# Kernel tuning notes

Hardware: AMD Instinct MI355X
Metric: run time of the kernel (lower is better)

The kernel has to match this reference:

```python
import jax, jax.numpy as jnp
import numpy as np

EMB = 1024

def setup_inputs() -> dict:
    key = jax.random.key(0)
    ks = jax.random.split(key, 6)
    B, S, E = 4, 2048, EMB
    x = jax.random.normal(ks[0], (B, S, E), dtype=jnp.float32)
    attention_mask = jax.random.randint(ks[1], (B, S, S), 0, 2, dtype=jnp.int32)
    proj_w = jax.random.normal(ks[2], (E, 3 * E), dtype=jnp.float32) * (1.0 / np.sqrt(E))
    proj_b = jax.random.normal(ks[3], (3 * E,), dtype=jnp.float32) * 0.02
    out_w = jax.random.normal(ks[4], (E, E), dtype=jnp.float32) * (1.0 / np.sqrt(E))
    out_b = jax.random.normal(ks[5], (E,), dtype=jnp.float32) * 0.02
    return {"x": x, "attention_mask": attention_mask, "proj_w": proj_w,
            "proj_b": proj_b, "out_w": out_w, "out_b": out_b}

def reference(x, attention_mask, proj_w, proj_b, out_w, out_b):
    E = x.shape[-1]
    scale = 1.0 / jnp.sqrt(jnp.asarray(E, x.dtype))
    qkv = x @ proj_w + proj_b                      # [B,S,3E]
    q, k, v = jnp.split(qkv, 3, axis=-1)           # each [B,S,E]
    scores = jnp.einsum('bqe,bke->bqk', q, k) * scale  # [B,S,S]
    scores = jnp.where(attention_mask == 0, jnp.asarray(-1e20, scores.dtype), scores)
    attn = jax.nn.softmax(scores, axis=-1)
    ctx = jnp.einsum('bqk,bke->bqe', attn, v)      # [B,S,E]
    return ctx @ out_w + out_b
```

## Files before the change

kernel.cpp:

```cpp
#include <hip/hip_runtime.h>
#include <cstdint>

typedef unsigned short u16;
typedef uint32_t u32;
typedef __bf16 bf16x8 __attribute__((ext_vector_type(8)));
typedef float f32x4 __attribute__((ext_vector_type(4)));

__device__ __forceinline__ u16 f2bf(float f) {
  unsigned u = __float_as_uint(f);
  u += 0x7fffu + ((u >> 16) & 1u);
  return (u16)(u >> 16);
}

__device__ __forceinline__ void async16(const void* g, void* l) {
  __builtin_amdgcn_global_load_lds(
      (const __attribute__((address_space(1))) uint32_t*)g,
      (__attribute__((address_space(3))) uint32_t*)l, 16, 0, 0);
}

__global__ __launch_bounds__(256) void k_prep(const float* __restrict__ x, u16* __restrict__ xb,
                                              const float* __restrict__ pw, u16* __restrict__ wt,
                                              const float* __restrict__ ow, u16* __restrict__ owt,
                                              const int* __restrict__ mask, u32* __restrict__ mbits) {
  const int bid = blockIdx.x;
  if (bid < 8192) {
    const int i = bid * 256 + threadIdx.x;
    const float4 v = ((const float4*)x)[i];
    ushort4 o;
    o.x = f2bf(v.x); o.y = f2bf(v.y); o.z = f2bf(v.z); o.w = f2bf(v.w);
    ((ushort4*)xb)[i] = o;
    return;
  }
  if (bid >= 12288) {
    const size_t w = (size_t)(bid - 12288) * 256 + threadIdx.x;
    const int* p = mask + w * 32;
    u32 bits = 0;
#pragma unroll
    for (int j = 0; j < 8; ++j) {
      const int4 v = ((const int4*)p)[j];
      bits |= (u32)(v.x & 1) << (j * 4 + 0);
      bits |= (u32)(v.y & 1) << (j * 4 + 1);
      bits |= (u32)(v.z & 1) << (j * 4 + 2);
      bits |= (u32)(v.w & 1) << (j * 4 + 3);
    }
    mbits[w] = bits;
    return;
  }
  __shared__ u16 tile[32][33];
  const int tx = threadIdx.x & 31, ty = threadIdx.x >> 5;
  const float* in;
  u16* outp;
  int lda, ldo, c0, r0;
  if (bid < 11264) {
    const int id = bid - 8192;
    c0 = (id % 96) * 32; r0 = (id / 96) * 32;
    in = pw; outp = wt; lda = 3072; ldo = 1024;
  } else {
    const int id = bid - 11264;
    c0 = (id % 32) * 32; r0 = (id / 32) * 32;
    in = ow; outp = owt; lda = 1024; ldo = 1024;
  }
#pragma unroll
  for (int i = 0; i < 4; ++i)
    tile[ty + i * 8][tx] = f2bf(in[(size_t)(r0 + ty + i * 8) * lda + c0 + tx]);
  __syncthreads();
#pragma unroll
  for (int i = 0; i < 4; ++i)
    outp[(size_t)(c0 + ty + i * 8) * ldo + r0 + tx] = tile[tx][ty + i * 8];
}

template <int MODE, int TM, int BN>
__device__ __forceinline__ void gemm_core(
    u16* As, u16* Bs,
    const u16* __restrict__ A, long lda, long bsA,
    const u16* __restrict__ Bt, long ldb, long bsB,
    void* __restrict__ C, long ldc, long bsC,
    int M, int N, int K,
    const float* __restrict__ bias, const u32* __restrict__ mbits,
    int b, int bx, int by) {
  constexpr int MT = TM / 32, NT = BN / 32;
  constexpr int ACALLS = TM / 8, TOT = (TM + BN) / 8, NC = TOT / 4;
  const int m0 = by * TM, n0 = bx * BN;
  const int lane = threadIdx.x & 63;
  const int w = threadIdx.x >> 6;
  const int wr = w >> 1, wc = w & 1;

  const int srow = lane >> 3;
  const int scol = ((lane & 7) ^ ((lane >> 3) & 7)) * 8;
  const u16* pa = A + (size_t)b * bsA + (size_t)(m0 + srow) * lda + scol;
  const u16* pb = Bt + (size_t)b * bsB + (size_t)(n0 + srow) * ldb + scol;

  const int m_l = lane & 15, q = lane >> 4, m7 = m_l & 7;
  const int offs[2] = {(q ^ m7) * 8, ((4 + q) ^ m7) * 8};

  f32x4 acc[MT][NT] = {};
  f32x4 accs[MT] = {};
  bf16x8 ones;
#pragma unroll
  for (int e = 0; e < 8; ++e) ones[e] = (__bf16)1.0f;

  for (int kt = 0; kt < K; kt += 64) {
    __syncthreads();
#pragma unroll
    for (int g = 0; g < NC; ++g) {
      const int idx = w * NC + g;
      if (idx < ACALLS)
        async16(pa + (size_t)(idx * 8) * lda, As + idx * 512);
      else
        async16(pb + (size_t)((idx - ACALLS) * 8) * ldb, Bs + (idx - ACALLS) * 512);
    }
    __syncthreads();
#pragma unroll
    for (int s = 0; s < 2; ++s) {
      bf16x8 af[MT], bfr[NT];
#pragma unroll
      for (int t = 0; t < MT; ++t)
        af[t] = *(const bf16x8*)(As + (wr * (TM / 2) + t * 16 + m_l) * 64 + offs[s]);
#pragma unroll
      for (int t = 0; t < NT; ++t)
        bfr[t] = *(const bf16x8*)(Bs + (wc * (BN / 2) + t * 16 + m_l) * 64 + offs[s]);
#pragma unroll
      for (int mt = 0; mt < MT; ++mt)
#pragma unroll
        for (int nt = 0; nt < NT; ++nt)
          acc[mt][nt] = __builtin_amdgcn_mfma_f32_16x16x32_bf16(af[mt], bfr[nt], acc[mt][nt], 0, 0, 0);
      if constexpr (MODE == 2) {
#pragma unroll
        for (int mt = 0; mt < MT; ++mt)
          accs[mt] = __builtin_amdgcn_mfma_f32_16x16x32_bf16(af[mt], ones, accs[mt], 0, 0, 0);
      }
    }
    pa += 64;
    pb += 64;
  }

  if constexpr (MODE == 1) {
    __syncthreads();
    const int rl = threadIdx.x >> 1, pr = threadIdx.x & 1;
    const uint2 v = *(const uint2*)(mbits + ((size_t)(b * M + m0 + rl)) * (N >> 5) + (n0 >> 5) + pr * 2);
    ((u32*)As)[rl * 4 + pr * 2] = v.x;
    ((u32*)As)[rl * 4 + pr * 2 + 1] = v.y;
    __syncthreads();
  }

  float rinv[MT][4];
  if constexpr (MODE == 2) {
#pragma unroll
    for (int mt = 0; mt < MT; ++mt)
#pragma unroll
      for (int r = 0; r < 4; ++r) rinv[mt][r] = 1.0f / accs[mt][r];
  }

#pragma unroll
  for (int mt = 0; mt < MT; ++mt) {
#pragma unroll
    for (int nt = 0; nt < NT; ++nt) {
      const int col = n0 + wc * (BN / 2) + nt * 16 + m_l;
      const int row0 = m0 + wr * (TM / 2) + mt * 16 + q * 4;
      if constexpr (MODE == 3) {
        ushort4 o;
        o.x = f2bf(acc[mt][nt][0]); o.y = f2bf(acc[mt][nt][1]);
        o.z = f2bf(acc[mt][nt][2]); o.w = f2bf(acc[mt][nt][3]);
        *(ushort4*)((u16*)C + (size_t)b * bsC + (size_t)col * ldc + row0) = o;
      } else {
#pragma unroll
        for (int r = 0; r < 4; ++r) {
          const int row = row0 + r;
          float v = acc[mt][nt][r];
          if constexpr (MODE == 0) {
            v += bias[col];
            if (col < 1024) v *= 0.03125f;
            ((u16*)C)[(size_t)b * bsC + (size_t)row * ldc + col] = f2bf(v);
          } else if constexpr (MODE == 1) {
            const int cl = wc * 64 + nt * 16 + m_l;
            const int rl = wr * 64 + mt * 16 + q * 4 + r;
            const u32 wb = ((const u32*)As)[rl * 4 + (cl >> 5)];
            v = ((wb >> (cl & 31)) & 1u) ? __expf(fminf(v, 30.f)) : 0.f;
            ((u16*)C)[(size_t)b * bsC + (size_t)row * ldc + col] = f2bf(v);
          } else if constexpr (MODE == 2) {
            v = v * rinv[mt][r] + bias[col];
            ((float*)C)[(size_t)b * bsC + (size_t)row * ldc + col] = v;
          }
        }
      }
    }
  }
}

template <int MODE, int TM, int BN>
__global__ __launch_bounds__(256) void gemm_bt(
    const u16* __restrict__ A, long lda, long bsA,
    const u16* __restrict__ Bt, long ldb, long bsB,
    void* __restrict__ C, long ldc, long bsC,
    int M, int N, int K,
    const float* __restrict__ bias, const u32* __restrict__ mbits) {
  __shared__ u16 As[TM * 64];
  __shared__ u16 Bs[BN * 64];
  const int gx = gridDim.x, gxy = gridDim.x * gridDim.y;
  const int T = gxy * gridDim.z;
  int L = blockIdx.x + gx * blockIdx.y + gxy * blockIdx.z;
  L = (L & 7) * (T >> 3) + (L >> 3);
  const int bz = L / gxy, r = L % gxy;
  gemm_core<MODE, TM, BN>(As, Bs, A, lda, bsA, Bt, ldb, bsB, C, ldc, bsC, M, N, K,
                          bias, mbits, bz, r % gx, r / gx);
}

extern "C" void kernel_launch(void* const* d_in, const int* in_sizes, int n_in,
                              void* d_out, int out_size, void* d_ws, size_t ws_size,
                              hipStream_t stream) {
  const float* x = (const float*)d_in[0];
  const int* mask = (const int*)d_in[1];
  const float* proj_w = (const float*)d_in[2];
  const float* proj_b = (const float*)d_in[3];
  const float* out_w = (const float*)d_in[4];
  const float* out_b = (const float*)d_in[5];
  float* out = (float*)d_out;

  char* ws = (char*)d_ws;
  u16* xb = (u16*)(ws);
  u16* wt = (u16*)(ws + 16777216);
  u16* owt = (u16*)(ws + 23068672);
  u16* qkv = (u16*)(ws + 25165824);
  u16* P = (u16*)(ws + 75497472);
  u32* mbits = (u32*)(ws + 109051904);
  u16* Ut = (u16*)xb;

  k_prep<<<14336, 256, 0, stream>>>(x, xb, proj_w, wt, out_w, owt, mask, mbits);
  gemm_bt<0, 128, 128><<<dim3(24, 64, 1), 256, 0, stream>>>(
      xb, 1024, 0, wt, 1024, 0, qkv, 3072, 0, 8192, 3072, 1024, proj_b, nullptr);
  gemm_bt<1, 128, 128><<<dim3(16, 16, 4), 256, 0, stream>>>(
      qkv, 3072, (long)2048 * 3072, qkv + 1024, 3072, (long)2048 * 3072,
      P, 2048, (long)2048 * 2048, 2048, 2048, 1024, nullptr, mbits);
  gemm_bt<3, 64, 128><<<dim3(8, 32, 4), 256, 0, stream>>>(
      qkv + 2048, 3072, (long)2048 * 3072, owt, 1024, 0,
      Ut, 2048, (long)1024 * 2048, 2048, 1024, 1024, nullptr, nullptr);
  gemm_bt<2, 128, 128><<<dim3(8, 16, 4), 256, 0, stream>>>(
      P, 2048, (long)2048 * 2048, Ut, 2048, (long)1024 * 2048,
      out, 1024, (long)2048 * 1024, 2048, 1024, 2048, out_b, nullptr);
}
```

Before: 331.7 us.

## Add 256x256 multi-stage pipelined GEMM for QKV projection and score kernels

```diff
diff --git a/kernel.cpp b/kernel.cpp
--- a/kernel.cpp
+++ b/kernel.cpp
@@ -67,6 +67,120 @@
 #pragma unroll
   for (int i = 0; i < 4; ++i)
     outp[(size_t)(c0 + ty + i * 8) * ldo + r0 + tx] = tile[tx][ty + i * 8];
+}
+
+template <int MODE>
+__global__ __launch_bounds__(512, 2) void gemm256(
+    const u16* __restrict__ A, long lda, long bsA,
+    const u16* __restrict__ Bt, long ldb, long bsB,
+    void* __restrict__ C, long ldc, long bsC,
+    int M, int N, int K,
+    const float* __restrict__ bias, const u32* __restrict__ mbits) {
+  __shared__ u16 sm[4][2][8192];
+  const int gx = gridDim.x, gxy = gridDim.x * gridDim.y;
+  const int T = gxy * gridDim.z;
+  int L = blockIdx.x + gx * blockIdx.y + gxy * blockIdx.z;
+  L = (L & 7) * (T >> 3) + (L >> 3);
+  const int b = L / gxy, rr = L % gxy, bx = rr % gx, by = rr / gx;
+  const int m0 = by * 256, n0 = bx * 256;
+  const int tid = threadIdx.x;
+  const int lane = tid & 63;
+  const int w = tid >> 6;
+  const int wr = w >> 2, wc = w & 3;
+
+  const int srow = tid >> 2;
+  const int sg = ((tid & 3) ^ (srow & 3)) * 8;
+  const u16* pa = A + (size_t)b * bsA + (size_t)(m0 + srow) * lda + sg;
+  const u16* pb = Bt + (size_t)b * bsB + (size_t)(n0 + srow) * ldb + sg;
+  const size_t a128 = (size_t)128 * lda, b128 = (size_t)128 * ldb;
+
+  const int m_l = lane & 15, q = lane >> 4;
+  const int xg = (q ^ (m_l & 3)) * 8;
+  const int aoff = (wr * 128 + m_l) * 32 + xg;
+  const int boff = (wc * 64 + m_l) * 32 + xg;
+
+  f32x4 acc[8][4] = {};
+
+#define STAGE(tt)                                   \
+  {                                                 \
+    const int bi_ = (tt)&3;                         \
+    const size_t ko_ = (size_t)(tt)*32;             \
+    u16* da_ = &sm[bi_][0][0] + tid * 8;            \
+    u16* db_ = &sm[bi_][1][0] + tid * 8;            \
+    async16(pa + ko_, da_);                         \
+    async16(pa + ko_ + a128, da_ + 4096);           \
+    async16(pb + ko_, db_);                         \
+    async16(pb + ko_ + b128, db_ + 4096);           \
+  }
+
+  const int NTL = K >> 5;
+  STAGE(0) STAGE(1) STAGE(2)
+  asm volatile("s_waitcnt vmcnt(8)" ::: "memory");
+  __builtin_amdgcn_s_barrier();
+
+  for (int t = 0; t < NTL; ++t) {
+    const u16* ab = &sm[t & 3][0][0] + aoff;
+    const u16* bb = &sm[t & 3][1][0] + boff;
+    bf16x8 af[8], bf[4];
+#pragma unroll
+    for (int mt = 0; mt < 8; ++mt) af[mt] = *(const bf16x8*)(ab + mt * 512);
+#pragma unroll
+    for (int nt = 0; nt < 4; ++nt) bf[nt] = *(const bf16x8*)(bb + nt * 512);
+    if (t + 3 < NTL) STAGE(t + 3)
+    __builtin_amdgcn_s_setprio(1);
+#pragma unroll
+    for (int mt = 0; mt < 8; ++mt)
+#pragma unroll
+      for (int nt = 0; nt < 4; ++nt)
+        acc[mt][nt] = __builtin_amdgcn_mfma_f32_16x16x32_bf16(af[mt], bf[nt], acc[mt][nt], 0, 0, 0);
+    __builtin_amdgcn_s_setprio(0);
+    __builtin_amdgcn_sched_barrier(0);
+    if (t + 3 < NTL)
+      asm volatile("s_waitcnt vmcnt(8)" ::: "memory");
+    else if (t + 3 == NTL)
+      asm volatile("s_waitcnt vmcnt(4)" ::: "memory");
+    else if (t + 2 == NTL)
+      asm volatile("s_waitcnt vmcnt(0)" ::: "memory");
+    if (t + 1 < NTL) __builtin_amdgcn_s_barrier();
+  }
+#undef STAGE
+
+  if constexpr (MODE == 1) {
+    __syncthreads();
+    u32* smw = (u32*)&sm[0][0][0];
+    const int rl = tid >> 1, wo = (tid & 1) * 4;
+    const uint4 mv = *(const uint4*)(mbits + ((size_t)b * M + m0 + rl) * (N >> 5) + (n0 >> 5) + wo);
+    smw[rl * 8 + wo] = mv.x;
+    smw[rl * 8 + wo + 1] = mv.y;
+    smw[rl * 8 + wo + 2] = mv.z;
+    smw[rl * 8 + wo + 3] = mv.w;
+    __syncthreads();
+  }
+
+#pragma unroll
+  for (int mt = 0; mt < 8; ++mt) {
+#pragma unroll
+    for (int nt = 0; nt < 4; ++nt) {
+      const int col = n0 + wc * 64 + nt * 16 + m_l;
+      const int row0 = m0 + wr * 128 + mt * 16 + q * 4;
+#pragma unroll
+      for (int r = 0; r < 4; ++r) {
+        const int row = row0 + r;
+        float v = acc[mt][nt][r];
+        if constexpr (MODE == 0) {
+          v += bias[col];
+          if (col < 1024) v *= 0.03125f;
+          ((u16*)C)[(size_t)b * bsC + (size_t)row * ldc + col] = f2bf(v);
+        } else {
+          const int cl = wc * 64 + nt * 16 + m_l;
+          const int rl2 = wr * 128 + mt * 16 + q * 4 + r;
+          const u32 wb = ((const u32*)&sm[0][0][0])[rl2 * 8 + (cl >> 5)];
+          v = ((wb >> (cl & 31)) & 1u) ? __expf(fminf(v, 30.f)) : 0.f;
+          ((u16*)C)[(size_t)b * bsC + (size_t)row * ldc + col] = f2bf(v);
+        }
+      }
+    }
+  }
 }
 
 template <int MODE, int TM, int BN>
@@ -134,15 +248,6 @@
     pb += 64;
   }
 
-  if constexpr (MODE == 1) {
-    __syncthreads();
-    const int rl = threadIdx.x >> 1, pr = threadIdx.x & 1;
-    const uint2 v = *(const uint2*)(mbits + ((size_t)(b * M + m0 + rl)) * (N >> 5) + (n0 >> 5) + pr * 2);
-    ((u32*)As)[rl * 4 + pr * 2] = v.x;
-    ((u32*)As)[rl * 4 + pr * 2 + 1] = v.y;
-    __syncthreads();
-  }
-
   float rinv[MT][4];
   if constexpr (MODE == 2) {
 #pragma unroll
@@ -167,17 +272,7 @@
         for (int r = 0; r < 4; ++r) {
           const int row = row0 + r;
           float v = acc[mt][nt][r];
-          if constexpr (MODE == 0) {
-            v += bias[col];
-            if (col < 1024) v *= 0.03125f;
-            ((u16*)C)[(size_t)b * bsC + (size_t)row * ldc + col] = f2bf(v);
-          } else if constexpr (MODE == 1) {
-            const int cl = wc * 64 + nt * 16 + m_l;
-            const int rl = wr * 64 + mt * 16 + q * 4 + r;
-            const u32 wb = ((const u32*)As)[rl * 4 + (cl >> 5)];
-            v = ((wb >> (cl & 31)) & 1u) ? __expf(fminf(v, 30.f)) : 0.f;
-            ((u16*)C)[(size_t)b * bsC + (size_t)row * ldc + col] = f2bf(v);
-          } else if constexpr (MODE == 2) {
+          if constexpr (MODE == 2) {
             v = v * rinv[mt][r] + bias[col];
             ((float*)C)[(size_t)b * bsC + (size_t)row * ldc + col] = v;
           }
@@ -226,9 +321,9 @@
   u16* Ut = (u16*)xb;
 
   k_prep<<<14336, 256, 0, stream>>>(x, xb, proj_w, wt, out_w, owt, mask, mbits);
-  gemm_bt<0, 128, 128><<<dim3(24, 64, 1), 256, 0, stream>>>(
+  gemm256<0><<<dim3(12, 32, 1), 512, 0, stream>>>(
       xb, 1024, 0, wt, 1024, 0, qkv, 3072, 0, 8192, 3072, 1024, proj_b, nullptr);
-  gemm_bt<1, 128, 128><<<dim3(16, 16, 4), 256, 0, stream>>>(
+  gemm256<1><<<dim3(8, 8, 4), 512, 0, stream>>>(
       qkv, 3072, (long)2048 * 3072, qkv + 1024, 3072, (long)2048 * 3072,
       P, 2048, (long)2048 * 2048, 2048, 2048, 1024, nullptr, mbits);
   gemm_bt<3, 64, 128><<<dim3(8, 32, 4), 256, 0, stream>>>(
```

Result: no change. 326.5 us (-1.6%).
